# Performance work log

Measured on AMD Instinct MI355X. Metric: run time of the kernel, lower is better.

Reference implementation:

```python
import jax, jax.numpy as jnp
import numpy as np

HIDDEN_DIM = 64  # self.hidden_dim = inc
N = 16384
C = 64


def setup_inputs() -> dict:
    key = jax.random.key(0)
    k1, k2, k3, k4, k5 = jax.random.split(key, 5)
    scale = 1.0 / np.sqrt(C)
    return {
        "hidden": jax.random.normal(k1, (N, C), dtype=jnp.float32),
        "query": jax.random.normal(k2, (N, C), dtype=jnp.float32),
        "Wq": jax.random.normal(k3, (C, C), dtype=jnp.float32) * scale,
        "Wk": jax.random.normal(k4, (C, C), dtype=jnp.float32) * scale,
        "Wv": jax.random.normal(k5, (C, C), dtype=jnp.float32) * scale,
    }


def reference(hidden, query, Wq, Wk, Wv):
    # Per-voxel linear projections (center-tap of the sparse 3x3x3 convs)
    q = query @ Wq            # [Nq, C]
    k = hidden @ Wk           # [Nk, C]
    v = hidden @ Wv           # [Nk, C]
    # score = q @ k.T / sqrt(hidden_dim)
    score = jnp.einsum("qc,kc->qk", q, k) / jnp.sqrt(jnp.float32(HIDDEN_DIM))
    attn = jax.nn.softmax(score, axis=-1)  # [Nq, Nk]
    weight = attn @ v         # [Nq, C] -> new hidden.F
    return weight
```

## Files before the change

### kernel.cpp

```cpp
#include <hip/hip_runtime.h>
#include <hip/hip_bf16.h>

#define NT 16384
#define CD 64

typedef __attribute__((ext_vector_type(8))) short bf16x8;
typedef __attribute__((ext_vector_type(16))) float f32x16;
typedef __attribute__((ext_vector_type(2))) int int2v;

#define AS1 __attribute__((address_space(1)))
#define AS3 __attribute__((address_space(3)))

__global__ __launch_bounds__(256) void proj_kernel(
    const float* __restrict__ hidden, const float* __restrict__ query,
    const float* __restrict__ Wq, const float* __restrict__ Wk, const float* __restrict__ Wv,
    __hip_bfloat16* __restrict__ qb, __hip_bfloat16* __restrict__ kb,
    __hip_bfloat16* __restrict__ vTb)
{
    __shared__ float qin[32][64];
    __shared__ float hin[32][64];
    const int tid = threadIdx.x;
    const int R0 = blockIdx.x * 32;
    {
        int r = tid >> 3, c0 = (tid & 7) * 8;
        const float4* qs = (const float4*)(query + (size_t)(R0 + r) * CD + c0);
        const float4* hs = (const float4*)(hidden + (size_t)(R0 + r) * CD + c0);
        *(float4*)&qin[r][c0]     = qs[0];
        *(float4*)&qin[r][c0 + 4] = qs[1];
        *(float4*)&hin[r][c0]     = hs[0];
        *(float4*)&hin[r][c0 + 4] = hs[1];
    }
    __syncthreads();
    const int c = tid & 63, rg = tid >> 6;
    const float SC = 0.18033688011112042f;
    float aq[8] = {0.f}, ak[8] = {0.f}, av[8] = {0.f};
    #pragma unroll 4
    for (int j = 0; j < 64; ++j) {
        float wq = Wq[j * 64 + c], wk = Wk[j * 64 + c], wv = Wv[j * 64 + c];
        #pragma unroll
        for (int r8 = 0; r8 < 8; ++r8) {
            float qv = qin[rg * 8 + r8][j];
            float hv = hin[rg * 8 + r8][j];
            aq[r8] += qv * wq;
            ak[r8] += hv * wk;
            av[r8] += hv * wv;
        }
    }
    #pragma unroll
    for (int r8 = 0; r8 < 8; ++r8) {
        int row = R0 + rg * 8 + r8;
        qb[(size_t)row * CD + c] = __float2bfloat16(aq[r8] * SC);
        kb[(size_t)row * CD + c] = __float2bfloat16(ak[r8]);
    }
    union { bf16x8 v; __hip_bfloat16 h[8]; } u;
    #pragma unroll
    for (int r8 = 0; r8 < 8; ++r8) u.h[r8] = __float2bfloat16(av[r8]);
    *(bf16x8*)(vTb + (size_t)c * NT + R0 + rg * 8) = u.v;
}

__device__ __forceinline__ void stage_tiles(
    char* kdst, char* vdst,
    const __hip_bfloat16* kb, const __hip_bfloat16* vTb,
    int kv, int wid, int lane)
{
    const char* kt = (const char*)(kb + (size_t)kv * CD);
    #pragma unroll
    for (int j = 0; j < 2; ++j) {
        int ob = (wid * 2 + j) * 1024;
        int o  = ob + lane * 16;
        int so = o ^ (((o >> 7) & 7) << 4);
        __builtin_amdgcn_global_load_lds((const AS1 void*)(kt + so),
                                         (AS3 void*)(kdst + ob), 16, 0, 0);
    }
    #pragma unroll
    for (int j = 0; j < 2; ++j) {
        int ob = (wid * 2 + j) * 1024;
        int o  = ob + lane * 16;
        int c  = o >> 7;
        int colb = (o & 127) ^ ((c & 7) << 4);
        __builtin_amdgcn_global_load_lds(
            (const AS1 void*)((const char*)vTb + ((size_t)c * NT + kv) * 2 + colb),
            (AS3 void*)(vdst + ob), 16, 0, 0);
    }
}

__device__ __forceinline__ void softpack_half(
    const f32x16& s, float& lsum, int paw[2][4])
{
    float p[16];
    #pragma unroll
    for (int r = 0; r < 16; ++r) p[r] = __builtin_amdgcn_exp2f(s[r]);
    {
        float t0 = ((p[0] + p[1]) + (p[2] + p[3])) + ((p[4] + p[5]) + (p[6] + p[7]));
        float t1 = ((p[8] + p[9]) + (p[10] + p[11])) + ((p[12] + p[13]) + (p[14] + p[15]));
        lsum += t0 + t1;
    }
    int w[8];
    #pragma unroll
    for (int r2 = 0; r2 < 4; ++r2)
        #pragma unroll
        for (int u = 0; u < 2; ++u)
            asm("v_cvt_pk_bf16_f32 %0, %1, %2"
                : "=v"(w[r2 * 2 + u]) : "v"(p[4*r2 + 2*u]), "v"(p[4*r2 + 2*u + 1]));
    #pragma unroll
    for (int r2e = 0; r2e < 4; r2e += 2)
        #pragma unroll
        for (int u = 0; u < 2; ++u) {
            int2v ra = __builtin_amdgcn_permlane32_swap(w[r2e*2 + u], w[(r2e+1)*2 + u], false, false);
            paw[r2e >> 1][u]     = ra.x;
            paw[r2e >> 1][2 + u] = ra.y;
        }
}

__global__ __launch_bounds__(256, 3) void flash_kernel(
    const __hip_bfloat16* __restrict__ qb, const __hip_bfloat16* __restrict__ kb,
    const __hip_bfloat16* __restrict__ vTb,
    __hip_bfloat16* __restrict__ part, float* __restrict__ lbuf, float* __restrict__ out,
    int nsplit, int kvlen)
{
    __shared__ __align__(16) char kbuf[3][8192];
    __shared__ __align__(16) char vbuf[3][8192];
    __shared__ float llds[4][32];

    const int tid  = threadIdx.x;
    const int lane = tid & 63, wid = tid >> 6;
    const int l31 = lane & 31, h = lane >> 5;
    const int split = blockIdx.x % nsplit;
    const int qblk  = blockIdx.x / nsplit;
    const int q0  = qblk * 128 + wid * 32;
    const int kv0 = split * kvlen;
    const int ntile = kvlen / 64;

    bf16x8 Qf[4];
    #pragma unroll
    for (int cc = 0; cc < 4; ++cc)
        Qf[cc] = *(const bf16x8*)(qb + (size_t)(q0 + l31) * CD + cc * 16 + h * 8);

    f32x16 acc[2];
    #pragma unroll
    for (int dt = 0; dt < 2; ++dt)
        #pragma unroll
        for (int r = 0; r < 16; ++r) acc[dt][r] = 0.f;
    float lsum = 0.f;

    const int krow0 = l31, krow1 = 32 + l31;
    const int kswz  = (l31 & 7) << 4;

    stage_tiles(kbuf[0], vbuf[0], kb, vTb, kv0, wid, lane);
    asm volatile("s_waitcnt vmcnt(0)" ::: "memory");
    __syncthreads();
    if (ntile > 1)
        stage_tiles(kbuf[1], vbuf[1], kb, vTb, kv0 + 64, wid, lane);

    f32x16 sP0, sP1;
    {
        f32x16 a0, a1;
        #pragma unroll
        for (int r = 0; r < 16; ++r) { a0[r] = 0.f; a1[r] = 0.f; }
        __builtin_amdgcn_s_setprio(1);
        #pragma unroll
        for (int cc = 0; cc < 4; ++cc) {
            int colb = (cc * 32 + h * 16) ^ kswz;
            bf16x8 k0 = *(const bf16x8*)(kbuf[0] + krow0 * 128 + colb);
            bf16x8 k1 = *(const bf16x8*)(kbuf[0] + krow1 * 128 + colb);
            a0 = __builtin_amdgcn_mfma_f32_32x32x16_bf16(k0, Qf[cc], a0, 0, 0, 0);
            a1 = __builtin_amdgcn_mfma_f32_32x32x16_bf16(k1, Qf[cc], a1, 0, 0, 0);
        }
        __builtin_amdgcn_s_setprio(0);
        sP0 = a0; sP1 = a1;
    }
    asm volatile("s_waitcnt vmcnt(0)" ::: "memory");
    __syncthreads();

    int prv = 0, cur = 1;
    for (int t = 1; t < ntile; ++t) {
        int nxt = cur + 1; if (nxt == 3) nxt = 0;
        if (t + 1 < ntile)
            stage_tiles(kbuf[nxt], vbuf[nxt], kb, vTb, kv0 + (t + 1) * 64, wid, lane);

        f32x16 sN0, sN1;
        #pragma unroll
        for (int r = 0; r < 16; ++r) { sN0[r] = 0.f; sN1[r] = 0.f; }
        const char* kbp = kbuf[cur];
        __builtin_amdgcn_s_setprio(1);
        #pragma unroll
        for (int cc = 0; cc < 4; ++cc) {
            int colb = (cc * 32 + h * 16) ^ kswz;
            bf16x8 k0 = *(const bf16x8*)(kbp + krow0 * 128 + colb);
            bf16x8 k1 = *(const bf16x8*)(kbp + krow1 * 128 + colb);
            sN0 = __builtin_amdgcn_mfma_f32_32x32x16_bf16(k0, Qf[cc], sN0, 0, 0, 0);
            sN1 = __builtin_amdgcn_mfma_f32_32x32x16_bf16(k1, Qf[cc], sN1, 0, 0, 0);
        }
        __builtin_amdgcn_s_setprio(0);

        int pa[2][4], pb[2][4];
        softpack_half(sP0, lsum, pa);
        softpack_half(sP1, lsum, pb);

        const char* vbp = vbuf[prv];
        __builtin_amdgcn_s_setprio(1);
        #pragma unroll
        for (int kc = 0; kc < 4; ++kc) {
            int colb = (kc * 32 + h * 16) ^ kswz;
            bf16x8 v0 = *(const bf16x8*)(vbp + krow0 * 128 + colb);
            bf16x8 v1 = *(const bf16x8*)(vbp + krow1 * 128 + colb);
            union { int i[4]; bf16x8 v; } pu;
            #pragma unroll
            for (int j = 0; j < 4; ++j) pu.i[j] = (kc < 2) ? pa[kc][j] : pb[kc - 2][j];
            acc[0] = __builtin_amdgcn_mfma_f32_32x32x16_bf16(pu.v, v0, acc[0], 0, 0, 0);
            acc[1] = __builtin_amdgcn_mfma_f32_32x32x16_bf16(pu.v, v1, acc[1], 0, 0, 0);
        }
        __builtin_amdgcn_s_setprio(0);

        sP0 = sN0; sP1 = sN1;
        asm volatile("s_waitcnt vmcnt(0)" ::: "memory");
        __syncthreads();
        prv = cur; cur = nxt;
    }

    {
        int pa[2][4], pb[2][4];
        softpack_half(sP0, lsum, pa);
        softpack_half(sP1, lsum, pb);
        const char* vbp = vbuf[prv];
        #pragma unroll
        for (int kc = 0; kc < 4; ++kc) {
            int colb = (kc * 32 + h * 16) ^ kswz;
            bf16x8 v0 = *(const bf16x8*)(vbp + krow0 * 128 + colb);
            bf16x8 v1 = *(const bf16x8*)(vbp + krow1 * 128 + colb);
            union { int i[4]; bf16x8 v; } pu;
            #pragma unroll
            for (int j = 0; j < 4; ++j) pu.i[j] = (kc < 2) ? pa[kc][j] : pb[kc - 2][j];
            acc[0] = __builtin_amdgcn_mfma_f32_32x32x16_bf16(pu.v, v0, acc[0], 0, 0, 0);
            acc[1] = __builtin_amdgcn_mfma_f32_32x32x16_bf16(pu.v, v1, acc[1], 0, 0, 0);
        }
    }

    float lfull = lsum + __shfl_xor(lsum, 32);

    if (nsplit == 1) {
        llds[wid][l31] = lfull;
        __builtin_amdgcn_wave_barrier();
        #pragma unroll
        for (int dt = 0; dt < 2; ++dt)
            #pragma unroll
            for (int r = 0; r < 16; ++r) {
                int qrow = (r & 3) + 8 * (r >> 2) + 4 * h;
                out[(size_t)(q0 + qrow) * CD + dt * 32 + l31] = acc[dt][r] / llds[wid][qrow];
            }
    } else {
        __hip_bfloat16* pb2 = part + ((size_t)split * NT + q0) * CD;
        #pragma unroll
        for (int dt = 0; dt < 2; ++dt)
            #pragma unroll
            for (int r = 0; r < 16; ++r) {
                int qrow = (r & 3) + 8 * (r >> 2) + 4 * h;
                pb2[qrow * CD + dt * 32 + l31] = __float2bfloat16(acc[dt][r]);
            }
        if (h == 0)
            lbuf[(size_t)split * NT + q0 + l31] = lfull;
    }
}

__global__ __launch_bounds__(256) void combine_kernel(
    const __hip_bfloat16* __restrict__ part, const float* __restrict__ lbuf,
    float* __restrict__ out, int S)
{
    const int tid = threadIdx.x;
    const int row = blockIdx.x * 4 + (tid >> 6);
    const int c = tid & 63;
    float L = 0.f, o = 0.f;
    for (int s = 0; s < S; ++s) {
        L += lbuf[(size_t)s * NT + row];
        o += __bfloat162float(part[((size_t)s * NT + row) * CD + c]);
    }
    out[(size_t)row * CD + c] = o / L;
}

extern "C" void kernel_launch(void* const* d_in, const int* in_sizes, int n_in,
                              void* d_out, int out_size, void* d_ws, size_t ws_size,
                              hipStream_t stream)
{
    (void)in_sizes; (void)n_in; (void)out_size;
    const float* hidden = (const float*)d_in[0];
    const float* query  = (const float*)d_in[1];
    const float* Wq = (const float*)d_in[2];
    const float* Wk = (const float*)d_in[3];
    const float* Wv = (const float*)d_in[4];
    float* out = (float*)d_out;

    char* ws = (char*)d_ws;
    __hip_bfloat16* qb  = (__hip_bfloat16*)ws;
    __hip_bfloat16* kb  = qb + (size_t)NT * CD;
    __hip_bfloat16* vTb = kb + (size_t)NT * CD;
    const size_t base = (size_t)3 * NT * CD * 2;
    const size_t per  = (size_t)NT * CD * 2 + (size_t)NT * 4;

    int S = 1;
    if (ws_size >= base + 16 * per) S = 16;
    else if (ws_size >= base + 8 * per) S = 8;
    else if (ws_size >= base + 4 * per) S = 4;
    else if (ws_size >= base + 2 * per) S = 2;

    __hip_bfloat16* part = (__hip_bfloat16*)(ws + base);
    float* lbuf = (float*)(ws + base + (size_t)S * NT * CD * 2);

    hipLaunchKernelGGL(proj_kernel, dim3(NT / 32), dim3(256), 0, stream,
                       hidden, query, Wq, Wk, Wv, qb, kb, vTb);
    hipLaunchKernelGGL(flash_kernel, dim3((NT / 128) * S), dim3(256), 0, stream,
                       qb, kb, vTb, part, lbuf, out, S, NT / S);
    if (S > 1)
        hipLaunchKernelGGL(combine_kernel, dim3(NT / 4), dim3(256), 0, stream,
                           part, lbuf, out, S);
}
```

Measured before the change: 112.6 us.

## Drop software-pipelined QK/PV skew and triple buffer to raise occupancy

```diff
diff --git a/kernel.cpp b/kernel.cpp
--- a/kernel.cpp
+++ b/kernel.cpp
@@ -112,15 +112,14 @@
         }
 }
 
-__global__ __launch_bounds__(256, 3) void flash_kernel(
+__global__ __launch_bounds__(256, 5) void flash_kernel(
     const __hip_bfloat16* __restrict__ qb, const __hip_bfloat16* __restrict__ kb,
     const __hip_bfloat16* __restrict__ vTb,
     __hip_bfloat16* __restrict__ part, float* __restrict__ lbuf, float* __restrict__ out,
     int nsplit, int kvlen)
 {
-    __shared__ __align__(16) char kbuf[3][8192];
-    __shared__ __align__(16) char vbuf[3][8192];
-    __shared__ float llds[4][32];
+    __shared__ __align__(16) char kbuf[2][8192];
+    __shared__ __align__(16) char vbuf[2][8192];
 
     const int tid  = threadIdx.x;
     const int lane = tid & 63, wid = tid >> 6;
@@ -149,61 +148,36 @@
     stage_tiles(kbuf[0], vbuf[0], kb, vTb, kv0, wid, lane);
     asm volatile("s_waitcnt vmcnt(0)" ::: "memory");
     __syncthreads();
-    if (ntile > 1)
-        stage_tiles(kbuf[1], vbuf[1], kb, vTb, kv0 + 64, wid, lane);
-
-    f32x16 sP0, sP1;
-    {
-        f32x16 a0, a1;
-        #pragma unroll
-        for (int r = 0; r < 16; ++r) { a0[r] = 0.f; a1[r] = 0.f; }
+
+    for (int t = 0; t < ntile; ++t) {
+        const int b = t & 1;
+        if (t + 1 < ntile)
+            stage_tiles(kbuf[b ^ 1], vbuf[b ^ 1], kb, vTb, kv0 + (t + 1) * 64, wid, lane);
+
+        f32x16 s0, s1;
+        #pragma unroll
+        for (int r = 0; r < 16; ++r) { s0[r] = 0.f; s1[r] = 0.f; }
         __builtin_amdgcn_s_setprio(1);
         #pragma unroll
         for (int cc = 0; cc < 4; ++cc) {
             int colb = (cc * 32 + h * 16) ^ kswz;
-            bf16x8 k0 = *(const bf16x8*)(kbuf[0] + krow0 * 128 + colb);
-            bf16x8 k1 = *(const bf16x8*)(kbuf[0] + krow1 * 128 + colb);
-            a0 = __builtin_amdgcn_mfma_f32_32x32x16_bf16(k0, Qf[cc], a0, 0, 0, 0);
-            a1 = __builtin_amdgcn_mfma_f32_32x32x16_bf16(k1, Qf[cc], a1, 0, 0, 0);
+            bf16x8 k0 = *(const bf16x8*)(kbuf[b] + krow0 * 128 + colb);
+            bf16x8 k1 = *(const bf16x8*)(kbuf[b] + krow1 * 128 + colb);
+            s0 = __builtin_amdgcn_mfma_f32_32x32x16_bf16(k0, Qf[cc], s0, 0, 0, 0);
+            s1 = __builtin_amdgcn_mfma_f32_32x32x16_bf16(k1, Qf[cc], s1, 0, 0, 0);
         }
         __builtin_amdgcn_s_setprio(0);
-        sP0 = a0; sP1 = a1;
-    }
-    asm volatile("s_waitcnt vmcnt(0)" ::: "memory");
-    __syncthreads();
-
-    int prv = 0, cur = 1;
-    for (int t = 1; t < ntile; ++t) {
-        int nxt = cur + 1; if (nxt == 3) nxt = 0;
-        if (t + 1 < ntile)
-            stage_tiles(kbuf[nxt], vbuf[nxt], kb, vTb, kv0 + (t + 1) * 64, wid, lane);
-
-        f32x16 sN0, sN1;
-        #pragma unroll
-        for (int r = 0; r < 16; ++r) { sN0[r] = 0.f; sN1[r] = 0.f; }
-        const char* kbp = kbuf[cur];
-        __builtin_amdgcn_s_setprio(1);
-        #pragma unroll
-        for (int cc = 0; cc < 4; ++cc) {
-            int colb = (cc * 32 + h * 16) ^ kswz;
-            bf16x8 k0 = *(const bf16x8*)(kbp + krow0 * 128 + colb);
-            bf16x8 k1 = *(const bf16x8*)(kbp + krow1 * 128 + colb);
-            sN0 = __builtin_amdgcn_mfma_f32_32x32x16_bf16(k0, Qf[cc], sN0, 0, 0, 0);
-            sN1 = __builtin_amdgcn_mfma_f32_32x32x16_bf16(k1, Qf[cc], sN1, 0, 0, 0);
-        }
-        __builtin_amdgcn_s_setprio(0);
 
         int pa[2][4], pb[2][4];
-        softpack_half(sP0, lsum, pa);
-        softpack_half(sP1, lsum, pb);
-
-        const char* vbp = vbuf[prv];
+        softpack_half(s0, lsum, pa);
+        softpack_half(s1, lsum, pb);
+
         __builtin_amdgcn_s_setprio(1);
         #pragma unroll
         for (int kc = 0; kc < 4; ++kc) {
             int colb = (kc * 32 + h * 16) ^ kswz;
-            bf16x8 v0 = *(const bf16x8*)(vbp + krow0 * 128 + colb);
-            bf16x8 v1 = *(const bf16x8*)(vbp + krow1 * 128 + colb);
+            bf16x8 v0 = *(const bf16x8*)(vbuf[b] + krow0 * 128 + colb);
+            bf16x8 v1 = *(const bf16x8*)(vbuf[b] + krow1 * 128 + colb);
             union { int i[4]; bf16x8 v; } pu;
             #pragma unroll
             for (int j = 0; j < 4; ++j) pu.i[j] = (kc < 2) ? pa[kc][j] : pb[kc - 2][j];
@@ -212,41 +186,21 @@
         }
         __builtin_amdgcn_s_setprio(0);
 
-        sP0 = sN0; sP1 = sN1;
         asm volatile("s_waitcnt vmcnt(0)" ::: "memory");
         __syncthreads();
-        prv = cur; cur = nxt;
-    }
-
-    {
-        int pa[2][4], pb[2][4];
-        softpack_half(sP0, lsum, pa);
-        softpack_half(sP1, lsum, pb);
-        const char* vbp = vbuf[prv];
-        #pragma unroll
-        for (int kc = 0; kc < 4; ++kc) {
-            int colb = (kc * 32 + h * 16) ^ kswz;
-            bf16x8 v0 = *(const bf16x8*)(vbp + krow0 * 128 + colb);
-            bf16x8 v1 = *(const bf16x8*)(vbp + krow1 * 128 + colb);
-            union { int i[4]; bf16x8 v; } pu;
-            #pragma unroll
-            for (int j = 0; j < 4; ++j) pu.i[j] = (kc < 2) ? pa[kc][j] : pb[kc - 2][j];
-            acc[0] = __builtin_amdgcn_mfma_f32_32x32x16_bf16(pu.v, v0, acc[0], 0, 0, 0);
-            acc[1] = __builtin_amdgcn_mfma_f32_32x32x16_bf16(pu.v, v1, acc[1], 0, 0, 0);
-        }
     }
 
     float lfull = lsum + __shfl_xor(lsum, 32);
 
     if (nsplit == 1) {
-        llds[wid][l31] = lfull;
-        __builtin_amdgcn_wave_barrier();
         #pragma unroll
         for (int dt = 0; dt < 2; ++dt)
             #pragma unroll
             for (int r = 0; r < 16; ++r) {
                 int qrow = (r & 3) + 8 * (r >> 2) + 4 * h;
-                out[(size_t)(q0 + qrow) * CD + dt * 32 + l31] = acc[dt][r] / llds[wid][qrow];
+                int li = __builtin_amdgcn_ds_bpermute(qrow * 4, __float_as_int(lfull));
+                out[(size_t)(q0 + qrow) * CD + dt * 32 + l31] =
+                    acc[dt][r] * __builtin_amdgcn_rcpf(__int_as_float(li));
             }
     } else {
         __hip_bfloat16* pb2 = part + ((size_t)split * NT + q0) * CD;
```

Result: slower. 165.9 us (+47.4%).
